# Optimization experiments

Measured on AMD Instinct MI355X. Metric: run time of the kernel, lower is better.

The kernel has to match this reference:

```python
import jax, jax.numpy as jnp
import numpy as np

NUM_LINKS = 4096
BUDGET = 100.0      # total_power_budget
PMAX = 0.1          # per_link_max
N_BISECT = 60       # bisection iterations (fp32 converges well before this)


def setup_inputs() -> dict:
    key = jax.random.key(0)
    raw_power = jax.random.normal(key, (8192, NUM_LINKS), dtype=jnp.float32)
    return {"raw_power": raw_power}


def _project(raw):
    """Euclidean projection of each row of raw onto {p : 0<=p<=PMAX, sum(p)<=BUDGET}.

    Closed-form water-filling: if clip(raw,0,PMAX) is feasible it is the answer;
    otherwise p = clip(raw - tau, 0, PMAX) with tau chosen so sum(p) = BUDGET
    (found by batched bisection + one implicit-function Newton correction,
    which also gives the exact QP-projection Jacobian).
    """
    clipped = jnp.clip(raw, 0.0, PMAX)
    feasible = jnp.sum(clipped, axis=-1, keepdims=True) <= BUDGET  # (B,1)

    raw_sg = jax.lax.stop_gradient(raw)
    lo = jnp.min(raw_sg, axis=-1, keepdims=True) - PMAX  # g(lo) = n*PMAX >= BUDGET
    hi = jnp.max(raw_sg, axis=-1, keepdims=True)         # g(hi) = 0

    def body(_, lohi):
        lo, hi = lohi
        mid = 0.5 * (lo + hi)
        g = jnp.sum(jnp.clip(raw_sg - mid, 0.0, PMAX), axis=-1, keepdims=True)
        too_big = g > BUDGET  # tau must increase
        return (jnp.where(too_big, mid, lo), jnp.where(too_big, hi, mid))

    lo, hi = jax.lax.fori_loop(0, N_BISECT, body, (lo, hi))
    tau0 = 0.5 * (lo + hi)  # (B,1), no gradient

    # Implicit-function (Newton) correction: g(tau) = sum(clip(raw-tau,0,PMAX)) = BUDGET.
    # dg/dtau = -n_active, dg/draw_i = active_i  => dtau/draw_i = active_i / n_active.
    active = (raw_sg - tau0 > 0.0) & (raw_sg - tau0 < PMAX)
    n_active = jnp.maximum(jnp.sum(active, axis=-1, keepdims=True).astype(raw.dtype), 1.0)
    g0 = jnp.sum(jnp.clip(raw - tau0, 0.0, PMAX), axis=-1, keepdims=True)
    tau = tau0 + (g0 - BUDGET) / n_active  # value ~= tau0, correct gradient

    p_budget = jnp.clip(raw - tau, 0.0, PMAX)
    return jnp.where(feasible, clipped, p_budget)


def reference(raw_power) -> jnp.ndarray:
    return _project(raw_power)
```

## Files before the change

### kernel.cpp

```cpp
#include <hip/hip_runtime.h>

#define NLINKS 4096
#define VEC 16

typedef float fvec4 __attribute__((ext_vector_type(4)));

constexpr float kPmax = 0.1f;
constexpr float kBudget = 100.0f;
constexpr int kGrid = 8;
constexpr int kFallbackIters = 8;

__device__ __forceinline__ float clip01(float x) {
  return __builtin_amdgcn_fmed3f(x, 0.0f, kPmax);
}

template <int N>
__device__ __forceinline__ void waveReduceSumN(float* x) {
#pragma unroll
  for (int m = 32; m >= 1; m >>= 1) {
    float t[N];
#pragma unroll
    for (int k = 0; k < N; ++k) t[k] = __shfl_xor(x[k], m, 64);
#pragma unroll
    for (int k = 0; k < N; ++k) x[k] += t[k];
  }
}
__device__ __forceinline__ float waveReduceMax(float x) {
#pragma unroll
  for (int m = 32; m >= 1; m >>= 1) x = fmaxf(x, __shfl_xor(x, m, 64));
  return x;
}

__device__ __forceinline__ void loadRow(const float* __restrict__ raw, int row,
                                        int lane, fvec4 (&v)[VEC]) {
  const fvec4* rp = (const fvec4*)(raw + (size_t)row * NLINKS);
#pragma unroll
  for (int j = 0; j < VEC; ++j) v[j] = __builtin_nontemporal_load(&rp[lane + 64 * j]);
}

__device__ __forceinline__ void processRow(const fvec4 (&v)[VEC],
                                           float* __restrict__ out, int row,
                                           int lane) {
  fvec4* op = (fvec4*)(out + (size_t)row * NLINKS);

  const float pts[kGrid] = {0.45f, 0.52f, 0.58f, 0.62f, 0.66f, 0.70f, 0.78f, 0.90f};

  float mx = -1e30f;
  float s[kGrid + 1];
#pragma unroll
  for (int k = 0; k <= kGrid; ++k) s[k] = 0.f;
#pragma unroll
  for (int j = 0; j < VEC; ++j) {
#pragma unroll
    for (int c = 0; c < 4; ++c) {
      const float x = v[j][c];
      mx = fmaxf(mx, x);
      s[0] += clip01(x);
#pragma unroll
      for (int i = 0; i < kGrid; ++i) s[i + 1] += clip01(x - pts[i]);
    }
  }
  waveReduceSumN<kGrid + 1>(s);
  mx = waveReduceMax(mx);
  const float fs = s[0];

  if (fs <= kBudget) {
#pragma unroll
    for (int j = 0; j < VEC; ++j) {
      fvec4 o;
#pragma unroll
      for (int c = 0; c < 4; ++c) o[c] = clip01(v[j][c]);
      __builtin_nontemporal_store(o, &op[lane + 64 * j]);
    }
    return;
  }

  float a = 0.f, ga = fs, b = mx, gb = 0.f;
  bool need_iter = true;
  if (s[1] < kBudget) {
    a = 0.f; ga = fs; b = pts[0]; gb = s[1];
  } else if (s[kGrid] > kBudget) {
    a = pts[kGrid - 1]; ga = s[kGrid]; b = mx; gb = 0.f;
  } else {
#pragma unroll
    for (int i = 0; i < kGrid - 1; ++i) {
      if (s[i + 1] >= kBudget && s[i + 2] <= kBudget) {
        a = pts[i]; ga = s[i + 1]; b = pts[i + 1]; gb = s[i + 2];
        need_iter = false;
        break;
      }
    }
  }

  if (need_iter) {
    int side = 0;
#pragma unroll 1
    for (int it = 0; it < kFallbackIters; ++it) {
      const float denom = gb - ga;
      float t = (denom != 0.f) ? b - (gb - kBudget) * (b - a) / denom
                               : 0.5f * (a + b);
      if (!(t > a && t < b)) t = 0.5f * (a + b);
      float s0 = 0.f, s1 = 0.f, s2 = 0.f, s3 = 0.f;
#pragma unroll
      for (int j = 0; j < VEC; ++j) {
        s0 += clip01(v[j].x - t);
        s1 += clip01(v[j].y - t);
        s2 += clip01(v[j].z - t);
        s3 += clip01(v[j].w - t);
      }
      float g = (s0 + s1) + (s2 + s3);
      waveReduceSumN<1>(&g);
      if (g > kBudget) {
        a = t; ga = g;
        if (side == 1) gb = kBudget + 0.5f * (gb - kBudget);
        side = 1;
      } else {
        b = t; gb = g;
        if (side == -1) ga = kBudget + 0.5f * (ga - kBudget);
        side = -1;
      }
    }
  }

  const float dd = ga - gb;
  float tau0 = (dd != 0.f) ? a + (ga - kBudget) * (b - a) / dd : 0.5f * (a + b);
  if (!(tau0 >= a && tau0 <= b)) tau0 = 0.5f * (a + b);

  float gn[2] = {0.f, 0.f};
#pragma unroll
  for (int j = 0; j < VEC; ++j) {
#pragma unroll
    for (int c = 0; c < 4; ++c) {
      const float t = v[j][c] - tau0;
      gn[0] += clip01(t);
      gn[1] += (t > 0.f && t < kPmax) ? 1.f : 0.f;
    }
  }
  waveReduceSumN<2>(gn);
  const float tau = tau0 + (gn[0] - kBudget) / fmaxf(gn[1], 1.0f);

#pragma unroll
  for (int j = 0; j < VEC; ++j) {
    fvec4 o;
#pragma unroll
    for (int c = 0; c < 4; ++c) o[c] = clip01(v[j][c] - tau);
    __builtin_nontemporal_store(o, &op[lane + 64 * j]);
  }
}

__global__ __launch_bounds__(256, 2) void proj_kernel(
    const float* __restrict__ raw, float* __restrict__ out, int rows) {
  const int wave = threadIdx.x >> 6;
  const int lane = threadIdx.x & 63;
  const int W = gridDim.x * 4;
  int r = blockIdx.x * 4 + wave;
  if (r >= rows) return;

  fvec4 vA[VEC], vB[VEC];
  loadRow(raw, r, lane, vA);

  while (true) {
    const int r1 = r + W;
    if (r1 < rows) loadRow(raw, r1, lane, vB);
    processRow(vA, out, r, lane);
    if (r1 >= rows) return;

    const int r2 = r1 + W;
    if (r2 < rows) loadRow(raw, r2, lane, vA);
    processRow(vB, out, r1, lane);
    if (r2 >= rows) return;
    r = r2;
  }
}

extern "C" void kernel_launch(void* const* d_in, const int* in_sizes, int n_in,
                              void* d_out, int out_size, void* d_ws, size_t ws_size,
                              hipStream_t stream) {
  const float* raw = (const float*)d_in[0];
  float* out = (float*)d_out;
  const int rows = in_sizes[0] / NLINKS;
  int blocks = (rows + 3) / 4;
  if (blocks > 512) blocks = 512;
  hipLaunchKernelGGL(proj_kernel, dim3(blocks), dim3(256), 0, stream,
                     raw, out, rows);
}
```

Baseline: 251.0 us.

## Prefetch next row via direct global-to-LDS loads instead of register double-buffer

Replaces the two-register-buffer row prefetch with global_load_lds transfers into a per-wave 16KB LDS slot. After the loads land, the row is copied into registers and the next row's load into the same slot is issued. This halves register pressure and drops the occupancy hint from launch_bounds. In exchange it adds 64KB of LDS per block, which limits blocks per CU, and an extra LDS read pass per row. The global_load_lds writes to the slot rely on manual waitcnt ordering rather than compiler-tracked dependencies.

```diff
diff --git a/kernel.cpp b/kernel.cpp
--- a/kernel.cpp
+++ b/kernel.cpp
@@ -31,11 +31,23 @@
   return x;
 }
 
-__device__ __forceinline__ void loadRow(const float* __restrict__ raw, int row,
-                                        int lane, fvec4 (&v)[VEC]) {
-  const fvec4* rp = (const fvec4*)(raw + (size_t)row * NLINKS);
+__device__ __forceinline__ void prefetchRow(const float* __restrict__ raw,
+                                            int row, int lane, float* slot) {
+  const float* rp = raw + (size_t)row * NLINKS;
 #pragma unroll
-  for (int j = 0; j < VEC; ++j) v[j] = __builtin_nontemporal_load(&rp[lane + 64 * j]);
+  for (int j = 0; j < VEC; ++j) {
+    __builtin_amdgcn_global_load_lds(
+        (__attribute__((address_space(1))) void*)(rp + 4 * (lane + 64 * j)),
+        (__attribute__((address_space(3))) void*)(slot + 256 * j),
+        16, 0, 0);
+  }
+}
+
+__device__ __forceinline__ void readRowLds(const float* slot, int lane,
+                                           fvec4 (&v)[VEC]) {
+  const fvec4* sp = (const fvec4*)slot;
+#pragma unroll
+  for (int j = 0; j < VEC; ++j) v[j] = sp[lane + 64 * j];
 }
 
 __device__ __forceinline__ void processRow(const fvec4 (&v)[VEC],
@@ -70,7 +82,7 @@
       fvec4 o;
 #pragma unroll
       for (int c = 0; c < 4; ++c) o[c] = clip01(v[j][c]);
-      __builtin_nontemporal_store(o, &op[lane + 64 * j]);
+      __builtin_nontemporal_store(o, &((fvec4*)op)[lane + 64 * j]);
     }
     return;
   }
@@ -144,32 +156,33 @@
     fvec4 o;
 #pragma unroll
     for (int c = 0; c < 4; ++c) o[c] = clip01(v[j][c] - tau);
-    __builtin_nontemporal_store(o, &op[lane + 64 * j]);
+    __builtin_nontemporal_store(o, &((fvec4*)op)[lane + 64 * j]);
   }
 }
 
-__global__ __launch_bounds__(256, 2) void proj_kernel(
+__global__ __launch_bounds__(256) void proj_kernel(
     const float* __restrict__ raw, float* __restrict__ out, int rows) {
+  __shared__ float lds[4 * NLINKS];
   const int wave = threadIdx.x >> 6;
   const int lane = threadIdx.x & 63;
+  float* slot = lds + wave * NLINKS;
   const int W = gridDim.x * 4;
   int r = blockIdx.x * 4 + wave;
   if (r >= rows) return;
 
-  fvec4 vA[VEC], vB[VEC];
-  loadRow(raw, r, lane, vA);
+  prefetchRow(raw, r, lane, slot);
 
+  fvec4 v[VEC];
   while (true) {
-    const int r1 = r + W;
-    if (r1 < rows) loadRow(raw, r1, lane, vB);
-    processRow(vA, out, r, lane);
-    if (r1 >= rows) return;
+    asm volatile("s_waitcnt vmcnt(0)" ::: "memory");
+    readRowLds(slot, lane, v);
+    asm volatile("s_waitcnt lgkmcnt(0)" ::: "memory");
 
-    const int r2 = r1 + W;
-    if (r2 < rows) loadRow(raw, r2, lane, vA);
-    processRow(vB, out, r1, lane);
-    if (r2 >= rows) return;
-    r = r2;
+    const int rn = r + W;
+    if (rn < rows) prefetchRow(raw, rn, lane, slot);
+    processRow(v, out, r, lane);
+    if (rn >= rows) return;
+    r = rn;
   }
 }
 
```

Result: faster. 241.3 us (-3.9%).
